# Performance work log

Hardware: AMD Instinct MI355X
Metric: run time of the kernel (lower is better)

The kernel has to match this reference:

```python
import jax, jax.numpy as jnp
import numpy as np

T, H, E, I, TOPK = 2048, 1024, 8, 2048, 2


def setup_inputs() -> dict:
    key = jax.random.key(0)
    k1, k2, k3, k4 = jax.random.split(key, 4)
    hidden_states = jax.random.normal(k1, (T, H), dtype=jnp.float32)
    router_logits = jax.random.normal(k2, (T, E), dtype=jnp.float32)
    # w13: merged gate+up projection [E, 2I, H]; w2: down projection [E, H, I]
    w13_weight = jax.random.normal(k3, (E, 2 * I, H), dtype=jnp.float32) * 0.02
    w2_weight = jax.random.normal(k4, (E, H, I), dtype=jnp.float32) * 0.02
    return {
        "hidden_states": hidden_states,
        "router_logits": router_logits,
        "w13_weight": w13_weight,
        "w2_weight": w2_weight,
        "top_k": TOPK,
    }


def reference(hidden_states, router_logits, w13_weight, w2_weight, top_k):
    num_experts = router_logits.shape[-1]
    # --- top-k routing (softmax -> top_k -> renormalize) ---
    probs = jax.nn.softmax(router_logits, axis=-1)           # [T, E]
    topk_w, topk_ids = jax.lax.top_k(probs, top_k)           # [T, K]
    topk_w = topk_w / jnp.sum(topk_w, axis=-1, keepdims=True)
    # per-token combine weight for each expert: [T, E]
    onehot = jax.nn.one_hot(topk_ids, num_experts, dtype=hidden_states.dtype)  # [T, K, E]
    combine_w = jnp.einsum("tk,tke->te", topk_w, onehot)
    # --- grouped expert GEMMs (gated SiLU MLP) ---
    gu = jnp.einsum("th,eih->tei", hidden_states, w13_weight)  # [T, E, 2I]
    inter = w13_weight.shape[1] // 2
    gate, up = gu[..., :inter], gu[..., inter:]
    act = jax.nn.silu(gate) * up                               # [T, E, I]
    y = jnp.einsum("tei,ehi->teh", act, w2_weight)             # [T, E, H]
    # --- combine ---
    out = jnp.einsum("teh,te->th", y, combine_w)               # [T, H]
    return out
```

## Files before the change

### kernel.cpp

```cpp
#include <hip/hip_runtime.h>

#define T_ 2048
#define H_ 1024
#define E_ 8
#define I_ 2048

typedef short bf16x8 __attribute__((ext_vector_type(8)));
typedef float f32x4 __attribute__((ext_vector_type(4)));
typedef unsigned short u16x8 __attribute__((ext_vector_type(8)));

__device__ __forceinline__ unsigned short f2bf(float f) {
  unsigned u = __builtin_bit_cast(unsigned, f);
  u += 0x7fffu + ((u >> 16) & 1u);
  return (unsigned short)(u >> 16);
}

#define GLOAD_LDS16(g, l)                                                     \
  __builtin_amdgcn_global_load_lds(                                           \
      (const __attribute__((address_space(1))) unsigned int*)(g),             \
      (__attribute__((address_space(3))) unsigned int*)(l), 16, 0, 0)

__global__ __launch_bounds__(256) void cvt_kernel(const float* __restrict__ s,
                                                  unsigned short* __restrict__ d,
                                                  int n8) {
  int i = blockIdx.x * blockDim.x + threadIdx.x;
  if (i >= n8) return;
  const float4* s4 = (const float4*)s;
  float4 a = s4[2 * i], b = s4[2 * i + 1];
  u16x8 v;
  v[0] = f2bf(a.x); v[1] = f2bf(a.y); v[2] = f2bf(a.z); v[3] = f2bf(a.w);
  v[4] = f2bf(b.x); v[5] = f2bf(b.y); v[6] = f2bf(b.z); v[7] = f2bf(b.w);
  *(u16x8*)(d + (size_t)i * 8) = v;
}

__global__ void router_kernel(const float* __restrict__ logits,
                              int* __restrict__ cnt,
                              int* __restrict__ plist,
                              float* __restrict__ wlist) {
  int t = blockIdx.x * blockDim.x + threadIdx.x;
  if (t >= T_) return;
  float l[E_];
#pragma unroll
  for (int e = 0; e < E_; ++e) l[e] = logits[t * E_ + e];
  int i0 = 0;
#pragma unroll
  for (int e = 1; e < E_; ++e) if (l[e] > l[i0]) i0 = e;
  int i1 = (i0 == 0) ? 1 : 0;
#pragma unroll
  for (int e = 0; e < E_; ++e) if (e != i0 && l[e] > l[i1]) i1 = e;
  float w1 = 1.f / (1.f + __expf(l[i0] - l[i1]));
  float w0 = 1.f - w1;
  int s0 = atomicAdd(&cnt[i0], 1);
  plist[i0 * T_ + s0] = 2 * t;
  wlist[i0 * T_ + s0] = w0;
  int s1 = atomicAdd(&cnt[i1], 1);
  plist[i1 * T_ + s1] = 2 * t + 1;
  wlist[i1 * T_ + s1] = w1;
}

__global__ __launch_bounds__(256, 4) void gemm1_kernel(
    const unsigned short* __restrict__ hs_bf,
    const float* __restrict__ w13,
    const int* __restrict__ cnt, const int* __restrict__ plist,
    const float* __restrict__ wlist, unsigned short* __restrict__ act) {
  const int bid = blockIdx.x;
  const int e = bid & 7;
  const int mt = (bid >> 3) & 15;
  const int nt = bid >> 7;
  const int M = cnt[e];
  if (mt * 128 >= M) return;
  const int Mrem = M - mt * 128;
  const int n0 = nt * 64;

  __shared__ __align__(16) unsigned short As[2][128][32];
  __shared__ __align__(16) unsigned short Bs[128][32];

  const int tid = threadIdx.x;
  const int lane = tid & 63;
  const int wid = tid >> 6;
  const int wm = (wid >> 1) * 64;
  const int wn = (wid & 1) * 32;

  const unsigned short* aSrc0;
  const unsigned short* aSrc1;
  {
    int cg = ((lane & 3) ^ ((lane >> 3) & 3)) * 8;
#pragma unroll
    for (int i = 0; i < 2; ++i) {
      int r = wid * 32 + i * 16 + (lane >> 2);
      int idx = mt * 128 + ((r < Mrem) ? r : 0);
      int p = plist[e * T_ + idx];
      const unsigned short* s = hs_bf + (size_t)(p >> 1) * H_ + cg;
      if (i == 0) aSrc0 = s; else aSrc1 = s;
    }
  }
  const int rb = wid * 32 + (lane >> 1);
  const int wrow = (rb < 64) ? (e * 2 * I_ + n0 + rb)
                             : (e * 2 * I_ + I_ + n0 + (rb - 64));
  const float* bSrc = w13 + (size_t)wrow * H_ + (lane & 1) * 16;
  const int fb = (rb >> 1) & 3;
  unsigned short* bDst0 = &Bs[rb][((((lane & 1) << 1) | 0) ^ fb) * 8];
  unsigned short* bDst1 = &Bs[rb][((((lane & 1) << 1) | 1) ^ fb) * 8];

  const int rda = ((lane >> 4) ^ ((lane >> 1) & 3)) * 8;
  const int l15 = lane & 15;

  f32x4 accg[4][2] = {};
  f32x4 accu[4][2] = {};

  GLOAD_LDS16(aSrc0, &As[0][wid * 32][0]);
  GLOAD_LDS16(aSrc1, &As[0][wid * 32 + 16][0]);
  float4 b0 = *(const float4*)(bSrc + 0);
  float4 b1 = *(const float4*)(bSrc + 4);
  float4 b2 = *(const float4*)(bSrc + 8);
  float4 b3 = *(const float4*)(bSrc + 12);

#pragma unroll 1
  for (int kt = 0; kt < 32; ++kt) {
    const int cur = kt & 1;
    asm volatile("s_waitcnt vmcnt(0)" ::: "memory");
    {
      u16x8 lo, hi;
      lo[0] = f2bf(b0.x); lo[1] = f2bf(b0.y); lo[2] = f2bf(b0.z); lo[3] = f2bf(b0.w);
      lo[4] = f2bf(b1.x); lo[5] = f2bf(b1.y); lo[6] = f2bf(b1.z); lo[7] = f2bf(b1.w);
      hi[0] = f2bf(b2.x); hi[1] = f2bf(b2.y); hi[2] = f2bf(b2.z); hi[3] = f2bf(b2.w);
      hi[4] = f2bf(b3.x); hi[5] = f2bf(b3.y); hi[6] = f2bf(b3.z); hi[7] = f2bf(b3.w);
      *(u16x8*)bDst0 = lo;
      *(u16x8*)bDst1 = hi;
    }
    if (kt + 1 < 32) {
      GLOAD_LDS16(aSrc0 + (kt + 1) * 32, &As[cur ^ 1][wid * 32][0]);
      GLOAD_LDS16(aSrc1 + (kt + 1) * 32, &As[cur ^ 1][wid * 32 + 16][0]);
      b0 = *(const float4*)(bSrc + (kt + 1) * 32 + 0);
      b1 = *(const float4*)(bSrc + (kt + 1) * 32 + 4);
      b2 = *(const float4*)(bSrc + (kt + 1) * 32 + 8);
      b3 = *(const float4*)(bSrc + (kt + 1) * 32 + 12);
    }
    asm volatile("s_waitcnt lgkmcnt(0)" ::: "memory");
    __builtin_amdgcn_s_barrier();
    __builtin_amdgcn_sched_barrier(0);

    bf16x8 bg[2], bu[2];
#pragma unroll
    for (int ni = 0; ni < 2; ++ni) {
      bg[ni] = *(const bf16x8*)&Bs[wn + ni * 16 + l15][rda];
      bu[ni] = *(const bf16x8*)&Bs[64 + wn + ni * 16 + l15][rda];
    }
#pragma unroll
    for (int mi = 0; mi < 4; ++mi) {
      bf16x8 af = *(const bf16x8*)&As[cur][wm + mi * 16 + l15][rda];
#pragma unroll
      for (int ni = 0; ni < 2; ++ni) {
        accg[mi][ni] = __builtin_amdgcn_mfma_f32_16x16x32_bf16(af, bg[ni], accg[mi][ni], 0, 0, 0);
        accu[mi][ni] = __builtin_amdgcn_mfma_f32_16x16x32_bf16(af, bu[ni], accu[mi][ni], 0, 0, 0);
      }
    }
    __builtin_amdgcn_sched_barrier(0);
    __builtin_amdgcn_s_barrier();
  }

  const int lrow = lane >> 4, lcol = lane & 15;
#pragma unroll
  for (int mi = 0; mi < 4; ++mi) {
#pragma unroll
    for (int r = 0; r < 4; ++r) {
      int rl = wm + mi * 16 + lrow * 4 + r;
      if (rl < Mrem) {
        int rr = mt * 128 + rl;
        int p = plist[e * T_ + rr];
        float w = wlist[e * T_ + rr];
        unsigned short* dst = act + (size_t)p * I_ + n0;
#pragma unroll
        for (int ni = 0; ni < 2; ++ni) {
          float g = accg[mi][ni][r];
          float u = accu[mi][ni][r];
          float a = (g / (1.f + __expf(-g))) * u * w;
          dst[wn + ni * 16 + lcol] = f2bf(a);
        }
      }
    }
  }
}

__global__ __launch_bounds__(256, 4) void gemm2_kernel(
    const unsigned short* __restrict__ act,
    const float* __restrict__ w2,
    const int* __restrict__ cnt, const int* __restrict__ plist,
    float* __restrict__ out) {
  const int bid = blockIdx.x;
  const int e = bid & 7;
  const int mt = (bid >> 3) & 15;
  const int nt = (bid >> 7) & 7;
  const int kb = bid >> 10;
  const int M = cnt[e];
  if (mt * 128 >= M) return;
  const int Mrem = M - mt * 128;
  const int n0 = nt * 128;
  const int k0 = kb * 512;

  __shared__ __align__(16) unsigned short As[2][128][32];
  __shared__ __align__(16) unsigned short Bs[128][32];

  const int tid = threadIdx.x;
  const int lane = tid & 63;
  const int wid = tid >> 6;
  const int wm = (wid >> 1) * 64;
  const int wn = (wid & 1) * 64;

  const unsigned short* aSrc0;
  const unsigned short* aSrc1;
  {
    int cg = ((lane & 3) ^ ((lane >> 3) & 3)) * 8;
#pragma unroll
    for (int i = 0; i < 2; ++i) {
      int r = wid * 32 + i * 16 + (lane >> 2);
      int idx = mt * 128 + ((r < Mrem) ? r : 0);
      int p = plist[e * T_ + idx];
      const unsigned short* s = act + (size_t)p * I_ + k0 + cg;
      if (i == 0) aSrc0 = s; else aSrc1 = s;
    }
  }
  const int rb = wid * 32 + (lane >> 1);
  const float* bSrc = w2 + ((size_t)e * H_ + n0 + rb) * I_ + k0 + (lane & 1) * 16;
  const int fb = (rb >> 1) & 3;
  unsigned short* bDst0 = &Bs[rb][((((lane & 1) << 1) | 0) ^ fb) * 8];
  unsigned short* bDst1 = &Bs[rb][((((lane & 1) << 1) | 1) ^ fb) * 8];

  const int rda = ((lane >> 4) ^ ((lane >> 1) & 3)) * 8;
  const int l15 = lane & 15;

  f32x4 acc[4][4] = {};

  GLOAD_LDS16(aSrc0, &As[0][wid * 32][0]);
  GLOAD_LDS16(aSrc1, &As[0][wid * 32 + 16][0]);
  float4 b0 = *(const float4*)(bSrc + 0);
  float4 b1 = *(const float4*)(bSrc + 4);
  float4 b2 = *(const float4*)(bSrc + 8);
  float4 b3 = *(const float4*)(bSrc + 12);

#pragma unroll 1
  for (int kt = 0; kt < 16; ++kt) {
    const int cur = kt & 1;
    asm volatile("s_waitcnt vmcnt(0)" ::: "memory");
    {
      u16x8 lo, hi;
      lo[0] = f2bf(b0.x); lo[1] = f2bf(b0.y); lo[2] = f2bf(b0.z); lo[3] = f2bf(b0.w);
      lo[4] = f2bf(b1.x); lo[5] = f2bf(b1.y); lo[6] = f2bf(b1.z); lo[7] = f2bf(b1.w);
      hi[0] = f2bf(b2.x); hi[1] = f2bf(b2.y); hi[2] = f2bf(b2.z); hi[3] = f2bf(b2.w);
      hi[4] = f2bf(b3.x); hi[5] = f2bf(b3.y); hi[6] = f2bf(b3.z); hi[7] = f2bf(b3.w);
      *(u16x8*)bDst0 = lo;
      *(u16x8*)bDst1 = hi;
    }
    if (kt + 1 < 16) {
      GLOAD_LDS16(aSrc0 + (kt + 1) * 32, &As[cur ^ 1][wid * 32][0]);
      GLOAD_LDS16(aSrc1 + (kt + 1) * 32, &As[cur ^ 1][wid * 32 + 16][0]);
      b0 = *(const float4*)(bSrc + (kt + 1) * 32 + 0);
      b1 = *(const float4*)(bSrc + (kt + 1) * 32 + 4);
      b2 = *(const float4*)(bSrc + (kt + 1) * 32 + 8);
      b3 = *(const float4*)(bSrc + (kt + 1) * 32 + 12);
    }
    asm volatile("s_waitcnt lgkmcnt(0)" ::: "memory");
    __builtin_amdgcn_s_barrier();
    __builtin_amdgcn_sched_barrier(0);

    bf16x8 bb[4];
#pragma unroll
    for (int ni = 0; ni < 4; ++ni)
      bb[ni] = *(const bf16x8*)&Bs[wn + ni * 16 + l15][rda];
#pragma unroll
    for (int mi = 0; mi < 4; ++mi) {
      bf16x8 af = *(const bf16x8*)&As[cur][wm + mi * 16 + l15][rda];
#pragma unroll
      for (int ni = 0; ni < 4; ++ni)
        acc[mi][ni] = __builtin_amdgcn_mfma_f32_16x16x32_bf16(af, bb[ni], acc[mi][ni], 0, 0, 0);
    }
    __builtin_amdgcn_sched_barrier(0);
    __builtin_amdgcn_s_barrier();
  }

  const int lrow = lane >> 4, lcol = lane & 15;
#pragma unroll
  for (int mi = 0; mi < 4; ++mi) {
#pragma unroll
    for (int r = 0; r < 4; ++r) {
      int rl = wm + mi * 16 + lrow * 4 + r;
      if (rl < Mrem) {
        int p = plist[e * T_ + mt * 128 + rl];
        int t = p >> 1;
#pragma unroll
        for (int ni = 0; ni < 4; ++ni)
          atomicAdd(&out[(size_t)t * H_ + n0 + wn + ni * 16 + lcol], acc[mi][ni][r]);
      }
    }
  }
}

extern "C" void kernel_launch(void* const* d_in, const int* in_sizes, int n_in,
                              void* d_out, int out_size, void* d_ws, size_t ws_size,
                              hipStream_t stream) {
  const float* hs     = (const float*)d_in[0];
  const float* logits = (const float*)d_in[1];
  const float* w13    = (const float*)d_in[2];
  const float* w2     = (const float*)d_in[3];
  float* out = (float*)d_out;

  char* ws = (char*)d_ws;
  size_t off = 0;
  int* cnt = (int*)(ws + off);           off += 256;
  int* plist = (int*)(ws + off);         off += (size_t)E_ * T_ * 4;
  float* wlist = (float*)(ws + off);     off += (size_t)E_ * T_ * 4;
  unsigned short* act = (unsigned short*)(ws + off);   off += (size_t)2 * T_ * I_ * 2;
  unsigned short* hs_bf = (unsigned short*)(ws + off); off += (size_t)T_ * H_ * 2;

  hipMemsetAsync(cnt, 0, 256, stream);
  hipMemsetAsync(d_out, 0, (size_t)out_size * sizeof(float), stream);

  const int nHs = T_ * H_ / 8;
  cvt_kernel<<<(nHs + 255) / 256, 256, 0, stream>>>(hs, hs_bf, nHs);
  router_kernel<<<T_ / 256, 256, 0, stream>>>(logits, cnt, plist, wlist);

  gemm1_kernel<<<E_ * 16 * 32, 256, 0, stream>>>(hs_bf, w13, cnt, plist, wlist, act);
  gemm2_kernel<<<E_ * 16 * 8 * 4, 256, 0, stream>>>(act, w2, cnt, plist, out);
}
```

Measured before the change: 217.0 us.

## Deepen gemm1 weight prefetch and replace gemm2 atomics with partial-sum reduction

gemm1 now keeps two sets of fp32 weight registers in flight, loading two K-steps ahead. It uses partial vmcnt waits instead of draining all loads every iteration, which is meant to hide global latency. gemm2 no longer does atomicAdd into the output. It writes per-split-K, per-slot partials to a 64MB workspace, and a new reduce kernel sums them, which also drops the output memset. This trades atomic contention for extra memory traffic and adds register pressure in gemm1.

After: 296.1 us. 36.5% more time.

```diff
diff --git a/kernel.cpp b/kernel.cpp
--- a/kernel.cpp
+++ b/kernel.cpp
@@ -71,6 +71,7 @@
   if (mt * 128 >= M) return;
   const int Mrem = M - mt * 128;
   const int n0 = nt * 64;
+  const int NT = 32;
 
   __shared__ __align__(16) unsigned short As[2][128][32];
   __shared__ __align__(16) unsigned short Bs[128][32];
@@ -108,34 +109,45 @@
   f32x4 accg[4][2] = {};
   f32x4 accu[4][2] = {};
 
+  float4 bset[2][4];
+
+#pragma unroll
+  for (int j = 0; j < 4; ++j) bset[0][j] = *(const float4*)(bSrc + j * 4);
   GLOAD_LDS16(aSrc0, &As[0][wid * 32][0]);
   GLOAD_LDS16(aSrc1, &As[0][wid * 32 + 16][0]);
-  float4 b0 = *(const float4*)(bSrc + 0);
-  float4 b1 = *(const float4*)(bSrc + 4);
-  float4 b2 = *(const float4*)(bSrc + 8);
-  float4 b3 = *(const float4*)(bSrc + 12);
-
-#pragma unroll 1
-  for (int kt = 0; kt < 32; ++kt) {
-    const int cur = kt & 1;
-    asm volatile("s_waitcnt vmcnt(0)" ::: "memory");
+#pragma unroll
+  for (int j = 0; j < 4; ++j) bset[1][j] = *(const float4*)(bSrc + 32 + j * 4);
+
+#pragma unroll 2
+  for (int kt = 0; kt < NT; ++kt) {
+    const int s = kt & 1;
+    if (kt + 1 < NT) asm volatile("s_waitcnt vmcnt(6)" ::: "memory");
+    else             asm volatile("s_waitcnt vmcnt(2)" ::: "memory");
     {
       u16x8 lo, hi;
-      lo[0] = f2bf(b0.x); lo[1] = f2bf(b0.y); lo[2] = f2bf(b0.z); lo[3] = f2bf(b0.w);
-      lo[4] = f2bf(b1.x); lo[5] = f2bf(b1.y); lo[6] = f2bf(b1.z); lo[7] = f2bf(b1.w);
-      hi[0] = f2bf(b2.x); hi[1] = f2bf(b2.y); hi[2] = f2bf(b2.z); hi[3] = f2bf(b2.w);
-      hi[4] = f2bf(b3.x); hi[5] = f2bf(b3.y); hi[6] = f2bf(b3.z); hi[7] = f2bf(b3.w);
+      lo[0] = f2bf(bset[s][0].x); lo[1] = f2bf(bset[s][0].y);
+      lo[2] = f2bf(bset[s][0].z); lo[3] = f2bf(bset[s][0].w);
+      lo[4] = f2bf(bset[s][1].x); lo[5] = f2bf(bset[s][1].y);
+      lo[6] = f2bf(bset[s][1].z); lo[7] = f2bf(bset[s][1].w);
+      hi[0] = f2bf(bset[s][2].x); hi[1] = f2bf(bset[s][2].y);
+      hi[2] = f2bf(bset[s][2].z); hi[3] = f2bf(bset[s][2].w);
+      hi[4] = f2bf(bset[s][3].x); hi[5] = f2bf(bset[s][3].y);
+      hi[6] = f2bf(bset[s][3].z); hi[7] = f2bf(bset[s][3].w);
       *(u16x8*)bDst0 = lo;
       *(u16x8*)bDst1 = hi;
     }
-    if (kt + 1 < 32) {
-      GLOAD_LDS16(aSrc0 + (kt + 1) * 32, &As[cur ^ 1][wid * 32][0]);
-      GLOAD_LDS16(aSrc1 + (kt + 1) * 32, &As[cur ^ 1][wid * 32 + 16][0]);
-      b0 = *(const float4*)(bSrc + (kt + 1) * 32 + 0);
-      b1 = *(const float4*)(bSrc + (kt + 1) * 32 + 4);
-      b2 = *(const float4*)(bSrc + (kt + 1) * 32 + 8);
-      b3 = *(const float4*)(bSrc + (kt + 1) * 32 + 12);
-    }
+    if (kt + 1 < NT) {
+      GLOAD_LDS16(aSrc0 + (kt + 1) * 32, &As[s ^ 1][wid * 32][0]);
+      GLOAD_LDS16(aSrc1 + (kt + 1) * 32, &As[s ^ 1][wid * 32 + 16][0]);
+    }
+    if (kt + 2 < NT) {
+#pragma unroll
+      for (int j = 0; j < 4; ++j)
+        bset[s][j] = *(const float4*)(bSrc + (kt + 2) * 32 + j * 4);
+    }
+    if (kt + 2 < NT)      asm volatile("s_waitcnt vmcnt(10)" ::: "memory");
+    else if (kt + 1 < NT) asm volatile("s_waitcnt vmcnt(6)" ::: "memory");
+    else                  asm volatile("s_waitcnt vmcnt(0)" ::: "memory");
     asm volatile("s_waitcnt lgkmcnt(0)" ::: "memory");
     __builtin_amdgcn_s_barrier();
     __builtin_amdgcn_sched_barrier(0);
@@ -148,7 +160,7 @@
     }
 #pragma unroll
     for (int mi = 0; mi < 4; ++mi) {
-      bf16x8 af = *(const bf16x8*)&As[cur][wm + mi * 16 + l15][rda];
+      bf16x8 af = *(const bf16x8*)&As[s][wm + mi * 16 + l15][rda];
 #pragma unroll
       for (int ni = 0; ni < 2; ++ni) {
         accg[mi][ni] = __builtin_amdgcn_mfma_f32_16x16x32_bf16(af, bg[ni], accg[mi][ni], 0, 0, 0);
@@ -186,7 +198,7 @@
     const unsigned short* __restrict__ act,
     const float* __restrict__ w2,
     const int* __restrict__ cnt, const int* __restrict__ plist,
-    float* __restrict__ out) {
+    float* __restrict__ part) {
   const int bid = blockIdx.x;
   const int e = bid & 7;
   const int mt = (bid >> 3) & 15;
@@ -286,13 +298,30 @@
       int rl = wm + mi * 16 + lrow * 4 + r;
       if (rl < Mrem) {
         int p = plist[e * T_ + mt * 128 + rl];
-        int t = p >> 1;
 #pragma unroll
         for (int ni = 0; ni < 4; ++ni)
-          atomicAdd(&out[(size_t)t * H_ + n0 + wn + ni * 16 + lcol], acc[mi][ni][r]);
+          part[((size_t)kb * 2 * T_ + p) * H_ + n0 + wn + ni * 16 + lcol] =
+              acc[mi][ni][r];
       }
     }
   }
+}
+
+__global__ __launch_bounds__(256) void reduce_kernel(const float* __restrict__ part,
+                                                     float* __restrict__ out) {
+  int i = blockIdx.x * blockDim.x + threadIdx.x;
+  int t = i >> 8;
+  int c = (i & 255) << 2;
+  f32x4 s = {0.f, 0.f, 0.f, 0.f};
+#pragma unroll
+  for (int kb = 0; kb < 4; ++kb) {
+#pragma unroll
+    for (int pp = 0; pp < 2; ++pp) {
+      f32x4 v = *(const f32x4*)(part + ((size_t)kb * 2 * T_ + 2 * t + pp) * H_ + c);
+      s += v;
+    }
+  }
+  *(f32x4*)(out + (size_t)t * H_ + c) = s;
 }
 
 extern "C" void kernel_launch(void* const* d_in, const int* in_sizes, int n_in,
@@ -311,14 +340,15 @@
   float* wlist = (float*)(ws + off);     off += (size_t)E_ * T_ * 4;
   unsigned short* act = (unsigned short*)(ws + off);   off += (size_t)2 * T_ * I_ * 2;
   unsigned short* hs_bf = (unsigned short*)(ws + off); off += (size_t)T_ * H_ * 2;
+  float* part = (float*)(ws + off);      off += (size_t)4 * 2 * T_ * H_ * 4;
 
   hipMemsetAsync(cnt, 0, 256, stream);
-  hipMemsetAsync(d_out, 0, (size_t)out_size * sizeof(float), stream);
 
   const int nHs = T_ * H_ / 8;
   cvt_kernel<<<(nHs + 255) / 256, 256, 0, stream>>>(hs, hs_bf, nHs);
   router_kernel<<<T_ / 256, 256, 0, stream>>>(logits, cnt, plist, wlist);
 
   gemm1_kernel<<<E_ * 16 * 32, 256, 0, stream>>>(hs_bf, w13, cnt, plist, wlist, act);
-  gemm2_kernel<<<E_ * 16 * 8 * 4, 256, 0, stream>>>(act, w2, cnt, plist, out);
-}
+  gemm2_kernel<<<E_ * 16 * 8 * 4, 256, 0, stream>>>(act, w2, cnt, plist, part);
+  reduce_kernel<<<T_ * H_ / 4 / 256, 256, 0, stream>>>(part, out);
+}
```

## Replace gemm2 atomic combine with bf16 partials and separate reduce kernel

Applied to the files above, without the earlier changes.

The down-projection GEMM drops from four split-K slices to two, and each block writes its tile as bf16 into a per-slot partial buffer instead of doing fp32 atomicAdd into the output. A new reduce kernel sums the two K-slices and two top-k slots per token into the output, which also removes the output memset. This avoids atomic contention and halves the number of weight-conversion passes per output tile. In exchange it adds an extra kernel launch, a partial-buffer write and read, and bf16 rounding of the partials before summation.

Measured after the change: 195.0 us. 1.11x faster.

```diff
diff --git a/kernel.cpp b/kernel.cpp
--- a/kernel.cpp
+++ b/kernel.cpp
@@ -13,6 +13,11 @@
   unsigned u = __builtin_bit_cast(unsigned, f);
   u += 0x7fffu + ((u >> 16) & 1u);
   return (unsigned short)(u >> 16);
+}
+
+__device__ __forceinline__ float bf2f(unsigned short h) {
+  unsigned u = ((unsigned)h) << 16;
+  return __builtin_bit_cast(float, u);
 }
 
 #define GLOAD_LDS16(g, l)                                                     \
@@ -186,7 +191,7 @@
     const unsigned short* __restrict__ act,
     const float* __restrict__ w2,
     const int* __restrict__ cnt, const int* __restrict__ plist,
-    float* __restrict__ out) {
+    unsigned short* __restrict__ part) {
   const int bid = blockIdx.x;
   const int e = bid & 7;
   const int mt = (bid >> 3) & 15;
@@ -196,7 +201,7 @@
   if (mt * 128 >= M) return;
   const int Mrem = M - mt * 128;
   const int n0 = nt * 128;
-  const int k0 = kb * 512;
+  const int k0 = kb * 1024;
 
   __shared__ __align__(16) unsigned short As[2][128][32];
   __shared__ __align__(16) unsigned short Bs[128][32];
@@ -239,7 +244,7 @@
   float4 b3 = *(const float4*)(bSrc + 12);
 
 #pragma unroll 1
-  for (int kt = 0; kt < 16; ++kt) {
+  for (int kt = 0; kt < 32; ++kt) {
     const int cur = kt & 1;
     asm volatile("s_waitcnt vmcnt(0)" ::: "memory");
     {
@@ -251,7 +256,7 @@
       *(u16x8*)bDst0 = lo;
       *(u16x8*)bDst1 = hi;
     }
-    if (kt + 1 < 16) {
+    if (kt + 1 < 32) {
       GLOAD_LDS16(aSrc0 + (kt + 1) * 32, &As[cur ^ 1][wid * 32][0]);
       GLOAD_LDS16(aSrc1 + (kt + 1) * 32, &As[cur ^ 1][wid * 32 + 16][0]);
       b0 = *(const float4*)(bSrc + (kt + 1) * 32 + 0);
@@ -286,13 +291,33 @@
       int rl = wm + mi * 16 + lrow * 4 + r;
       if (rl < Mrem) {
         int p = plist[e * T_ + mt * 128 + rl];
-        int t = p >> 1;
+        unsigned short* dst = part + ((size_t)kb * 2 * T_ + p) * H_ + n0 + wn + lcol;
 #pragma unroll
         for (int ni = 0; ni < 4; ++ni)
-          atomicAdd(&out[(size_t)t * H_ + n0 + wn + ni * 16 + lcol], acc[mi][ni][r]);
+          dst[ni * 16] = f2bf(acc[mi][ni][r]);
       }
     }
   }
+}
+
+__global__ __launch_bounds__(256) void reduce_kernel(const unsigned short* __restrict__ part,
+                                                     float* __restrict__ out) {
+  int i = blockIdx.x * blockDim.x + threadIdx.x;
+  int t = i >> 7;
+  int c = (i & 127) << 3;
+  float s[8] = {0.f, 0.f, 0.f, 0.f, 0.f, 0.f, 0.f, 0.f};
+#pragma unroll
+  for (int kb = 0; kb < 2; ++kb) {
+#pragma unroll
+    for (int pp = 0; pp < 2; ++pp) {
+      u16x8 v = *(const u16x8*)(part + ((size_t)kb * 2 * T_ + 2 * t + pp) * H_ + c);
+#pragma unroll
+      for (int j = 0; j < 8; ++j) s[j] += bf2f(v[j]);
+    }
+  }
+  float* o = out + (size_t)t * H_ + c;
+  *(f32x4*)o = *(f32x4*)&s[0];
+  *(f32x4*)(o + 4) = *(f32x4*)&s[4];
 }
 
 extern "C" void kernel_launch(void* const* d_in, const int* in_sizes, int n_in,
@@ -311,14 +336,15 @@
   float* wlist = (float*)(ws + off);     off += (size_t)E_ * T_ * 4;
   unsigned short* act = (unsigned short*)(ws + off);   off += (size_t)2 * T_ * I_ * 2;
   unsigned short* hs_bf = (unsigned short*)(ws + off); off += (size_t)T_ * H_ * 2;
+  unsigned short* part = (unsigned short*)(ws + off);  off += (size_t)2 * 2 * T_ * H_ * 2;
 
   hipMemsetAsync(cnt, 0, 256, stream);
-  hipMemsetAsync(d_out, 0, (size_t)out_size * sizeof(float), stream);
 
   const int nHs = T_ * H_ / 8;
   cvt_kernel<<<(nHs + 255) / 256, 256, 0, stream>>>(hs, hs_bf, nHs);
   router_kernel<<<T_ / 256, 256, 0, stream>>>(logits, cnt, plist, wlist);
 
   gemm1_kernel<<<E_ * 16 * 32, 256, 0, stream>>>(hs_bf, w13, cnt, plist, wlist, act);
-  gemm2_kernel<<<E_ * 16 * 8 * 4, 256, 0, stream>>>(act, w2, cnt, plist, out);
-}
+  gemm2_kernel<<<E_ * 16 * 8 * 2, 256, 0, stream>>>(act, w2, cnt, plist, part);
+  reduce_kernel<<<T_ * H_ / 8 / 256, 256, 0, stream>>>(part, out);
+}
```
